# Optimization experiments

Measured on AMD Instinct MI355X. Metric: run time of the kernel, lower is better.

Reference implementation:

```python
import jax, jax.numpy as jnp
from jax import lax
import numpy as np

E = 512        # embedding_dim (= rnn_first hidden, conv kernel, pool kernel)
VOCAB = 50000
H = 512        # hidden_dim of rnn_second
TEMP = 256     # Double_Linear out_feature
NL = 2         # num_layers (rnn_first layers == conv channels == second seq len)
NE = 2         # num_epoches (outer loop in forward)
T = 256        # sentence length
OUT = 1        # out_dim
PAD = (E - 1) // 2                       # 255
CONV_OUT = (E + 2 * PAD - (E - 1) - 1) // 2 + 1   # 256
POOL_OUT = (CONV_OUT + 2 * PAD - (E - 1) - 1) // 2 + 1  # 128 = rnn_second input


def _gru_scan(gi_all, h0, Whh, bhh):
    """PyTorch-convention GRU over precomputed input gates gi_all [T, 3H]."""
    def step(h, gi):
        gh = h @ Whh.T + bhh
        ir, iz, inn = jnp.split(gi, 3)
        hr, hz, hnn = jnp.split(gh, 3)
        r = jax.nn.sigmoid(ir + hr)
        z = jax.nn.sigmoid(iz + hz)
        n = jnp.tanh(inn + r * hnn)
        hn = (1.0 - z) * n + z * h
        return hn, hn
    return lax.scan(step, h0, gi_all)


def setup_inputs() -> dict:
    key = jax.random.key(0)
    ks = jax.random.split(key, 20)
    s = 0.05
    f32 = jnp.float32
    return {
        "sentA": jax.random.randint(ks[0], (T,), 0, VOCAB),
        "sentB": jax.random.randint(ks[1], (T,), 0, VOCAB),
        "emb": jax.random.normal(ks[2], (VOCAB, E), f32),
        "Wih1": jax.random.normal(ks[3], (NL, 3 * E, E), f32) * s,
        "Whh1": jax.random.normal(ks[4], (NL, 3 * E, E), f32) * s,
        "bih1": jax.random.normal(ks[5], (NL, 3 * E), f32) * s,
        "bhh1": jax.random.normal(ks[6], (NL, 3 * E), f32) * s,
        "conv_w": jax.random.normal(ks[7], (NL, NL, E), f32) * s,
        "conv_b": jax.random.normal(ks[8], (NL,), f32) * s,
        "Wih2": jax.random.normal(ks[9], (3 * H, POOL_OUT), f32) * s,
        "Whh2": jax.random.normal(ks[10], (3 * H, H), f32) * s,
        "bih2": jax.random.normal(ks[11], (3 * H,), f32) * s,
        "bhh2": jax.random.normal(ks[12], (3 * H,), f32) * s,
        "WA": jax.random.normal(ks[13], (H, TEMP), f32) * s,
        "WB": jax.random.normal(ks[14], (H, TEMP), f32) * s,
        "b_bi": jax.random.normal(ks[15], (TEMP,), f32) * s,
        "W_lin": jax.random.normal(ks[16], (OUT, TEMP), f32) * s,
        "b_lin": jax.random.normal(ks[17], (OUT,), f32) * s,
    }


def reference(sentA, sentB, emb, Wih1, Whh1, bih1, bhh1, conv_w, conv_b,
              Wih2, Whh2, bih2, bhh2, WA, WB, b_bi, W_lin, b_lin):
    dt = emb.dtype

    def encode(sent):
        h = emb[sent]                                   # [L, E]
        for _ in range(NE):                             # num_epoches loop
            x = h
            finals = []
            for l in range(NL):                         # stacked GRU layers
                gi = x @ Wih1[l].T + bih1[l]            # [L, 3E]
                hT, x = _gru_scan(gi, jnp.zeros((E,), dt), Whh1[l], bhh1[l])
                finals.append(hT)
            h = jnp.stack(finals)                       # hn: [NL, E] -> next seq
        # conv1d (in=out=NL channels, kernel E, stride 2) + maxpool1d
        y = lax.conv_general_dilated(h[None], conv_w, (2,), [(PAD, PAD)],
                                     dimension_numbers=("NCH", "OIH", "NCH"))
        y = y + conv_b[None, :, None]                   # [1, NL, CONV_OUT]
        y = lax.reduce_window(y, -jnp.inf, lax.max, (1, 1, E), (1, 1, 2),
                              [(0, 0), (0, 0), (PAD, PAD)])
        seq = y[0]                                      # [NL, POOL_OUT]
        gi2 = seq @ Wih2.T + bih2                       # [NL, 3H]
        hT, _ = _gru_scan(gi2, jnp.zeros((H,), dt), Whh2, bhh2)
        return hT                                       # [H]

    hA = encode(sentA)
    hB = encode(sentB)
    hx = hA * hB
    hv = jnp.abs(hA - hB)
    hs = hx @ WA + hv @ WB + b_bi                       # Double_Linear
    ht = jnp.tanh(hs)
    out = jax.nn.sigmoid(ht @ W_lin.T + b_lin)
    return out[None]                                    # [1, OUT]
```

## Files before the change

### kernel.cpp

```cpp
#include <hip/hip_runtime.h>
#include <math.h>


__device__ __forceinline__ float sigm(float x) { return 1.f / (1.f + expf(-x)); }

#define LDSP(k) ((k) + (((k) >> 4) << 2))

__device__ __forceinline__ float red32(float v) {
    v += __shfl_xor(v, 16, 64);
    v += __shfl_xor(v, 8, 64);
    v += __shfl_xor(v, 4, 64);
    v += __shfl_xor(v, 2, 64);
    v += __shfl_xor(v, 1, 64);
    return v;
}

__device__ __forceinline__ void poll_ge(const unsigned int* p, unsigned tgt) {
    unsigned v;
    do {
        v = __hip_atomic_load(p, __ATOMIC_RELAXED, __HIP_MEMORY_SCOPE_AGENT);
        if (v < tgt) __builtin_amdgcn_s_sleep(1);
    } while (v < tgt);
}

__device__ __forceinline__ void stage1024(float* dst, const float* src, int tid) {
    if (tid < 256) {
        const unsigned long long* s = (const unsigned long long*)src + tid * 2;
        unsigned long long d0 = __hip_atomic_load(s + 0, __ATOMIC_RELAXED,
                                                  __HIP_MEMORY_SCOPE_AGENT);
        unsigned long long d1 = __hip_atomic_load(s + 1, __ATOMIC_RELAXED,
                                                  __HIP_MEMORY_SCOPE_AGENT);
        union { unsigned long long u; float2 f; } c0, c1;
        c0.u = d0; c1.u = d1;
        float* d = dst + LDSP(tid * 4);
        d[0] = c0.f.x; d[1] = c0.f.y; d[2] = c1.f.x; d[3] = c1.f.y;
    }
}

__device__ __forceinline__ float gru1(float gr, float gz, float gn,
                                      float ar, float az, float an,
                                      const float bh[3], float hp) {
    float r = sigm(gr + ar + bh[0]);
    float z = sigm(gz + az + bh[1]);
    float n = tanhf(gn + r * (an + bh[2]));
    return (1.f - z) * n + z * hp;
}

__global__ __launch_bounds__(512, 1) void k_pipe(
    const float* __restrict__ Whh1, const float* __restrict__ bhh1,
    const float* __restrict__ Wih1, const float* __restrict__ bih1,
    const float* __restrict__ gi0,
    float* __restrict__ e2x,
    float* __restrict__ hbuf0,
    float* __restrict__ hbuf1,
    unsigned int* __restrict__ fL0,
    unsigned int* __restrict__ fL1)
{
    const int tid   = threadIdx.x;
    const int layer = blockIdx.x >> 5;
    const int wgi   = blockIdx.x & 31;
    const int grp   = tid >> 5;
    const int lane  = tid & 31;
    const int j     = wgi * 16 + grp;
    const int colbase = lane * 16;

    __shared__ float xlds[1280];
    __shared__ float hlds[1280];

    const size_t WS = (size_t)1536 * 512;
    const float* WH = Whh1 + (size_t)layer * WS;

    float wh[3][16];
#pragma unroll
    for (int q = 0; q < 3; ++q) {
        const float* src = WH + (size_t)(q * 512 + j) * 512 + colbase;
#pragma unroll
        for (int c4 = 0; c4 < 4; ++c4) {
            float4 v = *(const float4*)(src + c4 * 4);
            wh[q][c4*4+0] = v.x; wh[q][c4*4+1] = v.y;
            wh[q][c4*4+2] = v.z; wh[q][c4*4+3] = v.w;
        }
    }
#pragma unroll
    for (int q = 0; q < 3; ++q)
#pragma unroll
        for (int c = 0; c < 16; ++c)
            asm volatile("" : "+v"(wh[q][c]));

    float bh[3];
#pragma unroll
    for (int q = 0; q < 3; ++q) bh[q] = bhh1[layer * 1536 + q * 512 + j];

    float hprev[2] = {0.f, 0.f};

    if (layer == 0) {
        for (int t = 1; t <= 256; ++t) {
            float g0[3][2];
#pragma unroll
            for (int q = 0; q < 3; ++q)
#pragma unroll
                for (int s = 0; s < 2; ++s)
                    g0[q][s] = gi0[((size_t)(s * 256 + t - 1)) * 1536 + q * 512 + j];

            float acc[3][2] = {{0.f,0.f},{0.f,0.f},{0.f,0.f}};
            if (t > 1) {
                if (tid < 32) poll_ge(fL0 + tid * 16, (unsigned)(t - 1));
                __syncthreads();
                stage1024(xlds, hbuf0 + (size_t)(t - 1) * 1024, tid);
                __syncthreads();
#pragma unroll
                for (int s = 0; s < 2; ++s) {
                    const int base = s * 640 + 20 * lane;
#pragma unroll
                    for (int c4 = 0; c4 < 4; ++c4) {
                        float4 hv = *(const float4*)&xlds[base + c4 * 4];
#pragma unroll
                        for (int q = 0; q < 3; ++q)
                            acc[q][s] += wh[q][c4*4+0]*hv.x + wh[q][c4*4+1]*hv.y
                                       + wh[q][c4*4+2]*hv.z + wh[q][c4*4+3]*hv.w;
                    }
                }
#pragma unroll
                for (int q = 0; q < 3; ++q)
#pragma unroll
                    for (int s = 0; s < 2; ++s) acc[q][s] = red32(acc[q][s]);
            }

            float hn[2];
#pragma unroll
            for (int s = 0; s < 2; ++s) {
                hn[s] = gru1(g0[0][s], g0[1][s], g0[2][s],
                             acc[0][s], acc[1][s], acc[2][s], bh, hprev[s]);
                hprev[s] = hn[s];
            }
            if (lane == 0) {
#pragma unroll
                for (int s = 0; s < 2; ++s) {
                    __hip_atomic_store(hbuf0 + (size_t)t * 1024 + s * 512 + j, hn[s],
                                       __ATOMIC_RELAXED, __HIP_MEMORY_SCOPE_AGENT);
                    if (t == 256) e2x[s * 1024 + j] = hn[s];
                }
            }
            __builtin_amdgcn_s_waitcnt(0);
            __syncthreads();
            if (tid == 0)
                __hip_atomic_store(fL0 + wgi * 16, (unsigned)t,
                                   __ATOMIC_RELAXED, __HIP_MEMORY_SCOPE_AGENT);
        }
    } else {
        const float* WI = Wih1 + WS;
        float wi[3][16];
#pragma unroll
        for (int q = 0; q < 3; ++q) {
            const float* src = WI + (size_t)(q * 512 + j) * 512 + colbase;
#pragma unroll
            for (int c4 = 0; c4 < 4; ++c4) {
                float4 v = *(const float4*)(src + c4 * 4);
                wi[q][c4*4+0] = v.x; wi[q][c4*4+1] = v.y;
                wi[q][c4*4+2] = v.z; wi[q][c4*4+3] = v.w;
            }
        }
#pragma unroll
        for (int q = 0; q < 3; ++q)
#pragma unroll
            for (int c = 0; c < 16; ++c)
                asm volatile("" : "+v"(wi[q][c]));

        float bi[3];
#pragma unroll
        for (int q = 0; q < 3; ++q) bi[q] = bih1[1536 + q * 512 + j];

        for (int t = 1; t <= 256; ++t) {
            if (tid < 32) poll_ge(fL0 + tid * 16, (unsigned)t);
            else if (t > 1 && tid >= 64 && tid < 96)
                poll_ge(fL1 + (tid - 64) * 16, (unsigned)(t - 1));
            __syncthreads();
            stage1024(xlds, hbuf0 + (size_t)t * 1024, tid);
            if (t > 1 && tid >= 256 && tid < 512) {
                const int i = tid - 256;
                const unsigned long long* s =
                    (const unsigned long long*)(hbuf1 + (size_t)(t - 1) * 1024) + i * 2;
                unsigned long long d0 = __hip_atomic_load(s + 0, __ATOMIC_RELAXED,
                                                          __HIP_MEMORY_SCOPE_AGENT);
                unsigned long long d1 = __hip_atomic_load(s + 1, __ATOMIC_RELAXED,
                                                          __HIP_MEMORY_SCOPE_AGENT);
                union { unsigned long long u; float2 f; } c0, c1;
                c0.u = d0; c1.u = d1;
                float* d = hlds + LDSP(i * 4);
                d[0] = c0.f.x; d[1] = c0.f.y; d[2] = c1.f.x; d[3] = c1.f.y;
            }
            __syncthreads();

            float aR[2] = {0.f,0.f}, aZ[2] = {0.f,0.f};
            float aGN[2] = {0.f,0.f}, aHN[2] = {0.f,0.f};
#pragma unroll
            for (int s = 0; s < 2; ++s) {
                const int base = s * 640 + 20 * lane;
#pragma unroll
                for (int c4 = 0; c4 < 4; ++c4) {
                    float4 xv = *(const float4*)&xlds[base + c4 * 4];
                    aR[s]  += wi[0][c4*4+0]*xv.x + wi[0][c4*4+1]*xv.y
                            + wi[0][c4*4+2]*xv.z + wi[0][c4*4+3]*xv.w;
                    aZ[s]  += wi[1][c4*4+0]*xv.x + wi[1][c4*4+1]*xv.y
                            + wi[1][c4*4+2]*xv.z + wi[1][c4*4+3]*xv.w;
                    aGN[s] += wi[2][c4*4+0]*xv.x + wi[2][c4*4+1]*xv.y
                            + wi[2][c4*4+2]*xv.z + wi[2][c4*4+3]*xv.w;
                }
                if (t > 1) {
#pragma unroll
                    for (int c4 = 0; c4 < 4; ++c4) {
                        float4 hv = *(const float4*)&hlds[base + c4 * 4];
                        aR[s]  += wh[0][c4*4+0]*hv.x + wh[0][c4*4+1]*hv.y
                                + wh[0][c4*4+2]*hv.z + wh[0][c4*4+3]*hv.w;
                        aZ[s]  += wh[1][c4*4+0]*hv.x + wh[1][c4*4+1]*hv.y
                                + wh[1][c4*4+2]*hv.z + wh[1][c4*4+3]*hv.w;
                        aHN[s] += wh[2][c4*4+0]*hv.x + wh[2][c4*4+1]*hv.y
                                + wh[2][c4*4+2]*hv.z + wh[2][c4*4+3]*hv.w;
                    }
                }
            }
#pragma unroll
            for (int s = 0; s < 2; ++s) {
                aR[s] = red32(aR[s]); aZ[s] = red32(aZ[s]);
                aGN[s] = red32(aGN[s]); aHN[s] = red32(aHN[s]);
            }

            float hn[2];
#pragma unroll
            for (int s = 0; s < 2; ++s) {
                float r = sigm(aR[s] + bi[0] + bh[0]);
                float z = sigm(aZ[s] + bi[1] + bh[1]);
                float n = tanhf(aGN[s] + bi[2] + r * (aHN[s] + bh[2]));
                hn[s] = (1.f - z) * n + z * hprev[s];
                hprev[s] = hn[s];
            }
            if (lane == 0) {
#pragma unroll
                for (int s = 0; s < 2; ++s) {
                    __hip_atomic_store(hbuf1 + (size_t)t * 1024 + s * 512 + j, hn[s],
                                       __ATOMIC_RELAXED, __HIP_MEMORY_SCOPE_AGENT);
                    if (t == 256) e2x[s * 1024 + 512 + j] = hn[s];
                }
            }
            __builtin_amdgcn_s_waitcnt(0);
            __syncthreads();
            if (tid == 0)
                __hip_atomic_store(fL1 + wgi * 16, (unsigned)t,
                                   __ATOMIC_RELAXED, __HIP_MEMORY_SCOPE_AGENT);
        }
    }
}

__global__ __launch_bounds__(512, 1) void k_tail(
    const float* __restrict__ Wih1, const float* __restrict__ bih1,
    const float* __restrict__ Whh1, const float* __restrict__ bhh1,
    const float* __restrict__ convw, const float* __restrict__ convb,
    const float* __restrict__ Whh2, const float* __restrict__ bhh2,
    const float* __restrict__ bih2, const float* __restrict__ Srow,
    const float* __restrict__ e2x,
    const float* __restrict__ WA, const float* __restrict__ WB,
    const float* __restrict__ b_bi, const float* __restrict__ Wlin,
    const float* __restrict__ blin,
    float* __restrict__ tb0, float* __restrict__ tb1, float* __restrict__ tr,
    float* __restrict__ Mmax,
    unsigned int* __restrict__ tctr, unsigned int* __restrict__ mf,
    float* __restrict__ outp)
{
    const int tid = threadIdx.x;
    const int wgi = blockIdx.x;
    const int grp = tid >> 5, lane = tid & 31;
    const int j = wgi * 16 + grp, colbase = lane * 16;
    const size_t WS = (size_t)1536 * 512;

    __shared__ float xlds[1280];
    __shared__ float hlds[1280];
    __shared__ float red[8];
    __shared__ float smax[4];

#define WAIT_ALL(val)  do { if (tid < 32) poll_ge(tctr + tid * 16, (unsigned)(val)); \
                            __syncthreads(); } while (0)
#define PUBLISH(val)   do { __builtin_amdgcn_s_waitcnt(0); __syncthreads(); \
                            if (tid == 0) __hip_atomic_store(tctr + wgi * 16, (unsigned)(val), \
                                __ATOMIC_RELAXED, __HIP_MEMORY_SCOPE_AGENT); } while (0)

    if (tid < 256) {
        const int i = tid * 4, s = i >> 9, k = i & 511;
        float4 v = *(const float4*)(e2x + s * 1024 + k);
        float* d = xlds + LDSP(i);
        d[0] = v.x; d[1] = v.y; d[2] = v.z; d[3] = v.w;
    } else {
        const int i = (tid - 256) * 4, s = i >> 9, k = i & 511;
        float4 v = *(const float4*)(e2x + s * 1024 + 512 + k);
        float* d = hlds + LDSP(i);
        d[0] = v.x; d[1] = v.y; d[2] = v.z; d[3] = v.w;
    }
    __syncthreads();

    float gp[2][2][3];
    float bh[3], hp[2];
#pragma unroll
    for (int q = 0; q < 3; ++q) {
        const float* wp = Wih1 + (size_t)(q * 512 + j) * 512 + colbase;
        float w16[16];
#pragma unroll
        for (int c4 = 0; c4 < 4; ++c4) {
            float4 v = *(const float4*)(wp + c4 * 4);
            w16[c4*4+0] = v.x; w16[c4*4+1] = v.y; w16[c4*4+2] = v.z; w16[c4*4+3] = v.w;
        }
        float d00 = 0.f, d01 = 0.f, d10 = 0.f, d11 = 0.f;
#pragma unroll
        for (int c = 0; c < 16; ++c) {
            const int b0 = 20 * lane + ((colbase + c) & 15) + 0;
            (void)b0;
        }
#pragma unroll
        for (int c4 = 0; c4 < 4; ++c4) {
            float4 x0 = *(const float4*)&xlds[0 * 640 + 20 * lane + c4 * 4];
            float4 x1 = *(const float4*)&xlds[1 * 640 + 20 * lane + c4 * 4];
            float4 y0 = *(const float4*)&hlds[0 * 640 + 20 * lane + c4 * 4];
            float4 y1 = *(const float4*)&hlds[1 * 640 + 20 * lane + c4 * 4];
            d00 += w16[c4*4+0]*x0.x + w16[c4*4+1]*x0.y + w16[c4*4+2]*x0.z + w16[c4*4+3]*x0.w;
            d01 += w16[c4*4+0]*x1.x + w16[c4*4+1]*x1.y + w16[c4*4+2]*x1.z + w16[c4*4+3]*x1.w;
            d10 += w16[c4*4+0]*y0.x + w16[c4*4+1]*y0.y + w16[c4*4+2]*y0.z + w16[c4*4+3]*y0.w;
            d11 += w16[c4*4+0]*y1.x + w16[c4*4+1]*y1.y + w16[c4*4+2]*y1.z + w16[c4*4+3]*y1.w;
        }
        const float biq = bih1[q * 512 + j];
        gp[0][0][q] = red32(d00) + biq; gp[0][1][q] = red32(d01) + biq;
        gp[1][0][q] = red32(d10) + biq; gp[1][1][q] = red32(d11) + biq;
    }
#pragma unroll
    for (int q = 0; q < 3; ++q) bh[q] = bhh1[q * 512 + j];

#pragma unroll
    for (int s = 0; s < 2; ++s)
        hp[s] = gru1(gp[0][s][0], gp[0][s][1], gp[0][s][2], 0.f, 0.f, 0.f, bh, 0.f);
    if (lane == 0)
#pragma unroll
        for (int s = 0; s < 2; ++s)
            __hip_atomic_store(tb0 + 1024 + s * 512 + j, hp[s],
                               __ATOMIC_RELAXED, __HIP_MEMORY_SCOPE_AGENT);
    PUBLISH(1);

    WAIT_ALL(1);
    stage1024(hlds, tb0 + 1024, tid);
    __syncthreads();
    {
        float wh3[3][16];
#pragma unroll
        for (int q = 0; q < 3; ++q) {
            const float* wp = Whh1 + (size_t)(q * 512 + j) * 512 + colbase;
#pragma unroll
            for (int c4 = 0; c4 < 4; ++c4) {
                float4 v = *(const float4*)(wp + c4 * 4);
                wh3[q][c4*4+0] = v.x; wh3[q][c4*4+1] = v.y;
                wh3[q][c4*4+2] = v.z; wh3[q][c4*4+3] = v.w;
            }
        }
        float acc[3][2] = {{0.f,0.f},{0.f,0.f},{0.f,0.f}};
#pragma unroll
        for (int s = 0; s < 2; ++s) {
            const int base = s * 640 + 20 * lane;
#pragma unroll
            for (int c4 = 0; c4 < 4; ++c4) {
                float4 hv = *(const float4*)&hlds[base + c4 * 4];
#pragma unroll
                for (int q = 0; q < 3; ++q)
                    acc[q][s] += wh3[q][c4*4+0]*hv.x + wh3[q][c4*4+1]*hv.y
                               + wh3[q][c4*4+2]*hv.z + wh3[q][c4*4+3]*hv.w;
            }
        }
#pragma unroll
        for (int s = 0; s < 2; ++s) {
            float a0 = red32(acc[0][s]), a1 = red32(acc[1][s]), a2 = red32(acc[2][s]);
            hp[s] = gru1(gp[1][s][0], gp[1][s][1], gp[1][s][2], a0, a1, a2, bh, hp[s]);
        }
        if (lane == 0)
#pragma unroll
            for (int s = 0; s < 2; ++s)
                __hip_atomic_store(tb0 + 2048 + s * 512 + j, hp[s],
                                   __ATOMIC_RELAXED, __HIP_MEMORY_SCOPE_AGENT);
        PUBLISH(2);
    }

    WAIT_ALL(2);
    stage1024(xlds, tb0 + 1024, tid);
    if (tid >= 256) {
        const int i = tid - 256;
        const unsigned long long* s = (const unsigned long long*)(tb0 + 2048) + i * 2;
        unsigned long long d0 = __hip_atomic_load(s + 0, __ATOMIC_RELAXED, __HIP_MEMORY_SCOPE_AGENT);
        unsigned long long d1 = __hip_atomic_load(s + 1, __ATOMIC_RELAXED, __HIP_MEMORY_SCOPE_AGENT);
        union { unsigned long long u; float2 f; } c0, c1; c0.u = d0; c1.u = d1;
        float* d = hlds + LDSP(i * 4);
        d[0] = c0.f.x; d[1] = c0.f.y; d[2] = c1.f.x; d[3] = c1.f.y;
    }
    __syncthreads();
#pragma unroll
    for (int q = 0; q < 3; ++q) {
        const float* wp = Wih1 + WS + (size_t)(q * 512 + j) * 512 + colbase;
        float w16[16];
#pragma unroll
        for (int c4 = 0; c4 < 4; ++c4) {
            float4 v = *(const float4*)(wp + c4 * 4);
            w16[c4*4+0] = v.x; w16[c4*4+1] = v.y; w16[c4*4+2] = v.z; w16[c4*4+3] = v.w;
        }
        float d00 = 0.f, d01 = 0.f, d10 = 0.f, d11 = 0.f;
#pragma unroll
        for (int c4 = 0; c4 < 4; ++c4) {
            float4 x0 = *(const float4*)&xlds[0 * 640 + 20 * lane + c4 * 4];
            float4 x1 = *(const float4*)&xlds[1 * 640 + 20 * lane + c4 * 4];
            float4 y0 = *(const float4*)&hlds[0 * 640 + 20 * lane + c4 * 4];
            float4 y1 = *(const float4*)&hlds[1 * 640 + 20 * lane + c4 * 4];
            d00 += w16[c4*4+0]*x0.x + w16[c4*4+1]*x0.y + w16[c4*4+2]*x0.z + w16[c4*4+3]*x0.w;
            d01 += w16[c4*4+0]*x1.x + w16[c4*4+1]*x1.y + w16[c4*4+2]*x1.z + w16[c4*4+3]*x1.w;
            d10 += w16[c4*4+0]*y0.x + w16[c4*4+1]*y0.y + w16[c4*4+2]*y0.z + w16[c4*4+3]*y0.w;
            d11 += w16[c4*4+0]*y1.x + w16[c4*4+1]*y1.y + w16[c4*4+2]*y1.z + w16[c4*4+3]*y1.w;
        }
        const float biq = bih1[1536 + q * 512 + j];
        gp[0][0][q] = red32(d00) + biq; gp[0][1][q] = red32(d01) + biq;
        gp[1][0][q] = red32(d10) + biq; gp[1][1][q] = red32(d11) + biq;
    }
#pragma unroll
    for (int q = 0; q < 3; ++q) bh[q] = bhh1[1536 + q * 512 + j];

#pragma unroll
    for (int s = 0; s < 2; ++s)
        hp[s] = gru1(gp[0][s][0], gp[0][s][1], gp[0][s][2], 0.f, 0.f, 0.f, bh, 0.f);
    if (lane == 0)
#pragma unroll
        for (int s = 0; s < 2; ++s)
            __hip_atomic_store(tb1 + 1024 + s * 512 + j, hp[s],
                               __ATOMIC_RELAXED, __HIP_MEMORY_SCOPE_AGENT);
    PUBLISH(3);

    WAIT_ALL(3);
    stage1024(hlds, tb1 + 1024, tid);
    __syncthreads();
    {
        float wh3[3][16];
#pragma unroll
        for (int q = 0; q < 3; ++q) {
            const float* wp = Whh1 + WS + (size_t)(q * 512 + j) * 512 + colbase;
#pragma unroll
            for (int c4 = 0; c4 < 4; ++c4) {
                float4 v = *(const float4*)(wp + c4 * 4);
                wh3[q][c4*4+0] = v.x; wh3[q][c4*4+1] = v.y;
                wh3[q][c4*4+2] = v.z; wh3[q][c4*4+3] = v.w;
            }
        }
        float acc[3][2] = {{0.f,0.f},{0.f,0.f},{0.f,0.f}};
#pragma unroll
        for (int s = 0; s < 2; ++s) {
            const int base = s * 640 + 20 * lane;
#pragma unroll
            for (int c4 = 0; c4 < 4; ++c4) {
                float4 hv = *(const float4*)&hlds[base + c4 * 4];
#pragma unroll
                for (int q = 0; q < 3; ++q)
                    acc[q][s] += wh3[q][c4*4+0]*hv.x + wh3[q][c4*4+1]*hv.y
                               + wh3[q][c4*4+2]*hv.z + wh3[q][c4*4+3]*hv.w;
            }
        }
#pragma unroll
        for (int s = 0; s < 2; ++s) {
            float a0 = red32(acc[0][s]), a1 = red32(acc[1][s]), a2 = red32(acc[2][s]);
            hp[s] = gru1(gp[1][s][0], gp[1][s][1], gp[1][s][2], a0, a1, a2, bh, hp[s]);
        }
        if (lane == 0)
#pragma unroll
            for (int s = 0; s < 2; ++s)
                __hip_atomic_store(tb1 + 2048 + s * 512 + j, hp[s],
                                   __ATOMIC_RELAXED, __HIP_MEMORY_SCOPE_AGENT);
        PUBLISH(4);
    }

    WAIT_ALL(4);
    float m4[4];
    if (wgi == 0) {
        stage1024(xlds, tb0 + 2048, tid);
        if (tid >= 256) {
            const int i = tid - 256;
            const unsigned long long* s = (const unsigned long long*)(tb1 + 2048) + i * 2;
            unsigned long long d0 = __hip_atomic_load(s + 0, __ATOMIC_RELAXED, __HIP_MEMORY_SCOPE_AGENT);
            unsigned long long d1 = __hip_atomic_load(s + 1, __ATOMIC_RELAXED, __HIP_MEMORY_SCOPE_AGENT);
            union { unsigned long long u; float2 f; } c0, c1; c0.u = d0; c1.u = d1;
            float* d = hlds + LDSP(i * 4);
            d[0] = c0.f.x; d[1] = c0.f.y; d[2] = c1.f.x; d[3] = c1.f.y;
        }
        __syncthreads();
        for (int so = 0; so < 4; ++so) {
            const int s = so >> 1, o = so & 1;
            float acc = -3.4e38f;
            if (tid < 256) {
                acc = convb[o];
                const int base = 2 * tid - 255;
                for (int k = 0; k < 512; ++k) {
                    const int pos = base + k;
                    if ((unsigned)pos < 512u) {
                        const int gi0i = s * 512 + pos;
                        acc += xlds[LDSP(gi0i)] * convw[(size_t)(o * 2 + 0) * 512 + k]
                             + hlds[LDSP(gi0i)] * convw[(size_t)(o * 2 + 1) * 512 + k];
                    }
                }
            }
            float m = acc;
            m = fmaxf(m, __shfl_xor(m, 32, 64));
            m = fmaxf(m, __shfl_xor(m, 16, 64));
            m = fmaxf(m, __shfl_xor(m, 8, 64));
            m = fmaxf(m, __shfl_xor(m, 4, 64));
            m = fmaxf(m, __shfl_xor(m, 2, 64));
            m = fmaxf(m, __shfl_xor(m, 1, 64));
            if ((tid & 63) == 0) red[tid >> 6] = m;
            __syncthreads();
            if (tid == 0) {
                float mm = red[0];
                for (int i = 1; i < 8; ++i) mm = fmaxf(mm, red[i]);
                smax[so] = mm;
            }
            __syncthreads();
        }
        if (tid == 0) {
            for (int i = 0; i < 4; ++i)
                __hip_atomic_store(Mmax + i, smax[i],
                                   __ATOMIC_RELAXED, __HIP_MEMORY_SCOPE_AGENT);
            __builtin_amdgcn_s_waitcnt(0);
            __hip_atomic_store(mf, 1u, __ATOMIC_RELAXED, __HIP_MEMORY_SCOPE_AGENT);
        }
        __syncthreads();
#pragma unroll
        for (int i = 0; i < 4; ++i) m4[i] = smax[i];
    } else {
        if (tid == 0) poll_ge(mf, 1u);
        __syncthreads();
#pragma unroll
        for (int i = 0; i < 4; ++i)
            m4[i] = __hip_atomic_load((const float*)Mmax + i, __ATOMIC_RELAXED,
                                      __HIP_MEMORY_SCOPE_AGENT);
    }

    {
        float wh3[3][16];
#pragma unroll
        for (int q = 0; q < 3; ++q) {
            const float* wp = Whh2 + (size_t)(q * 512 + j) * 512 + colbase;
#pragma unroll
            for (int c4 = 0; c4 < 4; ++c4) {
                float4 v = *(const float4*)(wp + c4 * 4);
                wh3[q][c4*4+0] = v.x; wh3[q][c4*4+1] = v.y;
                wh3[q][c4*4+2] = v.z; wh3[q][c4*4+3] = v.w;
            }
        }
#pragma unroll
        for (int q = 0; q < 3; ++q) {
            const float sq = Srow[q * 512 + j];
            const float biq = bih2[q * 512 + j];
#pragma unroll
            for (int s = 0; s < 2; ++s) {
                gp[0][s][q] = m4[s * 2 + 0] * sq + biq;
                gp[1][s][q] = m4[s * 2 + 1] * sq + biq;
            }
            bh[q] = bhh2[q * 512 + j];
        }
#pragma unroll
        for (int s = 0; s < 2; ++s)
            hp[s] = gru1(gp[0][s][0], gp[0][s][1], gp[0][s][2], 0.f, 0.f, 0.f, bh, 0.f);
        if (lane == 0)
#pragma unroll
            for (int s = 0; s < 2; ++s)
                __hip_atomic_store(tr + 1024 + s * 512 + j, hp[s],
                                   __ATOMIC_RELAXED, __HIP_MEMORY_SCOPE_AGENT);
        PUBLISH(5);

        WAIT_ALL(5);
        stage1024(hlds, tr + 1024, tid);
        __syncthreads();
        float acc[3][2] = {{0.f,0.f},{0.f,0.f},{0.f,0.f}};
#pragma unroll
        for (int s = 0; s < 2; ++s) {
            const int base = s * 640 + 20 * lane;
#pragma unroll
            for (int c4 = 0; c4 < 4; ++c4) {
                float4 hv = *(const float4*)&hlds[base + c4 * 4];
#pragma unroll
                for (int q = 0; q < 3; ++q)
                    acc[q][s] += wh3[q][c4*4+0]*hv.x + wh3[q][c4*4+1]*hv.y
                               + wh3[q][c4*4+2]*hv.z + wh3[q][c4*4+3]*hv.w;
            }
        }
#pragma unroll
        for (int s = 0; s < 2; ++s) {
            float a0 = red32(acc[0][s]), a1 = red32(acc[1][s]), a2 = red32(acc[2][s]);
            hp[s] = gru1(gp[1][s][0], gp[1][s][1], gp[1][s][2], a0, a1, a2, bh, hp[s]);
        }
        if (lane == 0)
#pragma unroll
            for (int s = 0; s < 2; ++s)
                __hip_atomic_store(tr + 2048 + s * 512 + j, hp[s],
                                   __ATOMIC_RELAXED, __HIP_MEMORY_SCOPE_AGENT);
        PUBLISH(6);
    }

    WAIT_ALL(6);
    if (wgi != 0) return;
    stage1024(xlds, tr + 2048, tid);
    __syncthreads();
    float v = 0.f;
    if (tid < 256) {
        float acc = b_bi[tid];
        for (int jj = 0; jj < 512; ++jj) {
            const float a = xlds[LDSP(jj)];
            const float b = xlds[LDSP(512 + jj)];
            acc += (a * b) * WA[(size_t)jj * 256 + tid]
                 + fabsf(a - b) * WB[(size_t)jj * 256 + tid];
        }
        v = tanhf(acc) * Wlin[tid];
    }
    v += __shfl_xor(v, 32, 64);
    v += __shfl_xor(v, 16, 64);
    v += __shfl_xor(v, 8, 64);
    v += __shfl_xor(v, 4, 64);
    v += __shfl_xor(v, 2, 64);
    v += __shfl_xor(v, 1, 64);
    if ((tid & 63) == 0) red[tid >> 6] = v;
    __syncthreads();
    if (tid == 0) {
        float ssum = blin[0];
        for (int i = 0; i < 8; ++i) ssum += red[i];
        outp[0] = 1.f / (1.f + expf(-ssum));
    }
#undef WAIT_ALL
#undef PUBLISH
}

__global__ __launch_bounds__(256, 2) void k_gemm_gi(
    const float* __restrict__ W, const float* __restrict__ bias,
    const float* __restrict__ emb, const int* __restrict__ sentA,
    const int* __restrict__ sentB, float* __restrict__ out)
{
    __shared__ float At[32][68];
    __shared__ float Wt[32][68];
    const int tid = threadIdx.x;
    const int n0 = blockIdx.x * 64;
    const int m0 = blockIdx.y * 64;
    const int lrow = tid >> 3, lc4 = tid & 7;

    const int ma = m0 + lrow, mb = ma + 32;
    const int ia = (ma < 256) ? sentA[ma & 255] : sentB[ma & 255];
    const int ib = (mb < 256) ? sentA[mb & 255] : sentB[mb & 255];
    const float* ar0 = emb + (size_t)ia * 512;
    const float* ar1 = emb + (size_t)ib * 512;
    const float* wr0 = W + (size_t)(n0 + lrow) * 512;
    const float* wr1 = wr0 + (size_t)32 * 512;

    const int ty = tid >> 4, tx = tid & 15;
    float acc[4][4];
#pragma unroll
    for (int i = 0; i < 4; ++i)
#pragma unroll
        for (int jj = 0; jj < 4; ++jj) acc[i][jj] = 0.f;

    for (int kk = 0; kk < 512; kk += 32) {
        float4 a0 = *(const float4*)(ar0 + kk + lc4 * 4);
        float4 a1 = *(const float4*)(ar1 + kk + lc4 * 4);
        float4 w0 = *(const float4*)(wr0 + kk + lc4 * 4);
        float4 w1 = *(const float4*)(wr1 + kk + lc4 * 4);
        __syncthreads();
        const int kb = lc4 * 4;
        At[kb+0][lrow] = a0.x; At[kb+1][lrow] = a0.y; At[kb+2][lrow] = a0.z; At[kb+3][lrow] = a0.w;
        At[kb+0][lrow+32] = a1.x; At[kb+1][lrow+32] = a1.y; At[kb+2][lrow+32] = a1.z; At[kb+3][lrow+32] = a1.w;
        Wt[kb+0][lrow] = w0.x; Wt[kb+1][lrow] = w0.y; Wt[kb+2][lrow] = w0.z; Wt[kb+3][lrow] = w0.w;
        Wt[kb+0][lrow+32] = w1.x; Wt[kb+1][lrow+32] = w1.y; Wt[kb+2][lrow+32] = w1.z; Wt[kb+3][lrow+32] = w1.w;
        __syncthreads();
#pragma unroll
        for (int k = 0; k < 32; ++k) {
            float4 av = *(const float4*)&At[k][ty * 4];
            float4 wv = *(const float4*)&Wt[k][tx * 4];
            acc[0][0] += av.x * wv.x; acc[0][1] += av.x * wv.y; acc[0][2] += av.x * wv.z; acc[0][3] += av.x * wv.w;
            acc[1][0] += av.y * wv.x; acc[1][1] += av.y * wv.y; acc[1][2] += av.y * wv.z; acc[1][3] += av.y * wv.w;
            acc[2][0] += av.z * wv.x; acc[2][1] += av.z * wv.y; acc[2][2] += av.z * wv.z; acc[2][3] += av.z * wv.w;
            acc[3][0] += av.w * wv.x; acc[3][1] += av.w * wv.y; acc[3][2] += av.w * wv.z; acc[3][3] += av.w * wv.w;
        }
    }
    float4 b4 = *(const float4*)(bias + n0 + tx * 4);
#pragma unroll
    for (int i = 0; i < 4; ++i) {
        const int m = m0 + ty * 4 + i;
        float4 r;
        r.x = acc[i][0] + b4.x; r.y = acc[i][1] + b4.y;
        r.z = acc[i][2] + b4.z; r.w = acc[i][3] + b4.w;
        *(float4*)(out + (size_t)m * 1536 + n0 + tx * 4) = r;
    }
}

__global__ __launch_bounds__(256) void k_init(
    const float* __restrict__ Wih2, float* __restrict__ Srow,
    unsigned int* __restrict__ flags)
{
    const int g = blockIdx.x * 256 + threadIdx.x;
    if (g < 1536) {
        float s = 0.f;
        for (int k = 0; k < 128; ++k) s += Wih2[(size_t)g * 128 + k];
        Srow[g] = s;
    }
    if (g < 1552) flags[g] = 0u;
}

extern "C" void kernel_launch(void* const* d_in, const int* in_sizes, int n_in,
                              void* d_out, int out_size, void* d_ws, size_t ws_size,
                              hipStream_t stream)
{
    const int*   sentA = (const int*)d_in[0];
    const int*   sentB = (const int*)d_in[1];
    const float* emb   = (const float*)d_in[2];
    const float* Wih1  = (const float*)d_in[3];
    const float* Whh1  = (const float*)d_in[4];
    const float* bih1  = (const float*)d_in[5];
    const float* bhh1  = (const float*)d_in[6];
    const float* convw = (const float*)d_in[7];
    const float* convb = (const float*)d_in[8];
    const float* Wih2  = (const float*)d_in[9];
    const float* Whh2  = (const float*)d_in[10];
    const float* bih2  = (const float*)d_in[11];
    const float* bhh2  = (const float*)d_in[12];
    const float* WA    = (const float*)d_in[13];
    const float* WB    = (const float*)d_in[14];
    const float* b_bi  = (const float*)d_in[15];
    const float* Wlin  = (const float*)d_in[16];
    const float* blin  = (const float*)d_in[17];

    float* ws = (float*)d_ws;
    size_t off = 0;
    float* gi_buf = ws + off; off += 786432;
    float* e2x    = ws + off; off += 2048;
    float* hbuf0  = ws + off; off += 257 * 1024;
    float* hbuf1  = ws + off; off += 257 * 1024;
    float* tb0    = ws + off; off += 3 * 1024;
    float* tb1    = ws + off; off += 3 * 1024;
    float* tr     = ws + off; off += 3 * 1024;
    float* Mmax   = ws + off; off += 16;
    float* Srow   = ws + off; off += 1536;
    unsigned int* flags = (unsigned int*)(ws + off);
    unsigned int* fL0  = flags;
    unsigned int* fL1  = flags + 512;
    unsigned int* tctr = flags + 1024;
    unsigned int* mf   = flags + 1536;

    k_init<<<8, 256, 0, stream>>>(Wih2, Srow, flags);

    k_gemm_gi<<<dim3(24, 8), 256, 0, stream>>>(Wih1, bih1, emb, sentA, sentB, gi_buf);

    k_pipe<<<64, 512, 0, stream>>>(Whh1, bhh1, Wih1, bih1, gi_buf,
                                   e2x, hbuf0, hbuf1, fL0, fL1);

    k_tail<<<32, 512, 0, stream>>>(Wih1, bih1, Whh1, bhh1, convw, convb,
                                   Whh2, bhh2, bih2, Srow, e2x,
                                   WA, WB, b_bi, Wlin, blin,
                                   tb0, tb1, tr, Mmax, tctr, mf, (float*)d_out);
}
```

Measured before the change: 1.360 ms.

## Replace flag-based sync with poisoned-value polling and fuse input GEMM into pipeline

Removes the separate input-gate GEMM kernel: layer 0 now gathers embedding rows and computes its input projection inline using register-resident Wih weights, as layer 1 already did. Per-step flag counters and their extra barriers are replaced by polling the hidden-state buffers directly until no element holds a poison sentinel, which k_init now writes over both buffers. LDS staging is double-buffered so only one barrier per step is needed. Layer 0 does more work per step, and correctness now depends on no computed hidden value ever equalling the sentinel bit pattern (2.0f, which a GRU hidden state bounded in (-1,1) cannot reach).

```diff
diff --git a/kernel.cpp b/kernel.cpp
--- a/kernel.cpp
+++ b/kernel.cpp
@@ -3,6 +3,8 @@
 
 
 __device__ __forceinline__ float sigm(float x) { return 1.f / (1.f + expf(-x)); }
+
+#define POISON_U32 0x40000000u
 
 #define LDSP(k) ((k) + (((k) >> 4) << 2))
 
@@ -21,6 +23,25 @@
         v = __hip_atomic_load(p, __ATOMIC_RELAXED, __HIP_MEMORY_SCOPE_AGENT);
         if (v < tgt) __builtin_amdgcn_s_sleep(1);
     } while (v < tgt);
+}
+
+__device__ __forceinline__ void stage4_poison(float* dstbase, const float* src,
+                                              int idx) {
+    const unsigned long long* sp = (const unsigned long long*)src + idx * 2;
+    unsigned long long d0, d1;
+    for (;;) {
+        d0 = __hip_atomic_load(sp + 0, __ATOMIC_RELAXED, __HIP_MEMORY_SCOPE_AGENT);
+        d1 = __hip_atomic_load(sp + 1, __ATOMIC_RELAXED, __HIP_MEMORY_SCOPE_AGENT);
+        if ((unsigned)(d0 & 0xFFFFFFFFu) != POISON_U32 &&
+            (unsigned)(d0 >> 32)         != POISON_U32 &&
+            (unsigned)(d1 & 0xFFFFFFFFu) != POISON_U32 &&
+            (unsigned)(d1 >> 32)         != POISON_U32) break;
+        __builtin_amdgcn_s_sleep(1);
+    }
+    union { unsigned long long u; float2 f; } c0, c1;
+    c0.u = d0; c1.u = d1;
+    float* d = dstbase + LDSP(idx * 4);
+    d[0] = c0.f.x; d[1] = c0.f.y; d[2] = c1.f.x; d[3] = c1.f.y;
 }
 
 __device__ __forceinline__ void stage1024(float* dst, const float* src, int tid) {
@@ -49,12 +70,11 @@
 __global__ __launch_bounds__(512, 1) void k_pipe(
     const float* __restrict__ Whh1, const float* __restrict__ bhh1,
     const float* __restrict__ Wih1, const float* __restrict__ bih1,
-    const float* __restrict__ gi0,
+    const float* __restrict__ emb,
+    const int* __restrict__ sentA, const int* __restrict__ sentB,
     float* __restrict__ e2x,
     float* __restrict__ hbuf0,
-    float* __restrict__ hbuf1,
-    unsigned int* __restrict__ fL0,
-    unsigned int* __restrict__ fL1)
+    float* __restrict__ hbuf1)
 {
     const int tid   = threadIdx.x;
     const int layer = blockIdx.x >> 5;
@@ -64,189 +84,116 @@
     const int j     = wgi * 16 + grp;
     const int colbase = lane * 16;
 
-    __shared__ float xlds[1280];
-    __shared__ float hlds[1280];
+    __shared__ float xl[2][1280];
+    __shared__ float hl[2][1280];
 
     const size_t WS = (size_t)1536 * 512;
     const float* WH = Whh1 + (size_t)layer * WS;
-
-    float wh[3][16];
+    const float* WI = Wih1 + (size_t)layer * WS;
+
+    float wh[3][16], wi[3][16];
 #pragma unroll
     for (int q = 0; q < 3; ++q) {
-        const float* src = WH + (size_t)(q * 512 + j) * 512 + colbase;
+        const float* srcH = WH + (size_t)(q * 512 + j) * 512 + colbase;
+        const float* srcI = WI + (size_t)(q * 512 + j) * 512 + colbase;
 #pragma unroll
         for (int c4 = 0; c4 < 4; ++c4) {
-            float4 v = *(const float4*)(src + c4 * 4);
-            wh[q][c4*4+0] = v.x; wh[q][c4*4+1] = v.y;
-            wh[q][c4*4+2] = v.z; wh[q][c4*4+3] = v.w;
+            float4 vH = *(const float4*)(srcH + c4 * 4);
+            float4 vI = *(const float4*)(srcI + c4 * 4);
+            wh[q][c4*4+0] = vH.x; wh[q][c4*4+1] = vH.y;
+            wh[q][c4*4+2] = vH.z; wh[q][c4*4+3] = vH.w;
+            wi[q][c4*4+0] = vI.x; wi[q][c4*4+1] = vI.y;
+            wi[q][c4*4+2] = vI.z; wi[q][c4*4+3] = vI.w;
         }
     }
 #pragma unroll
     for (int q = 0; q < 3; ++q)
 #pragma unroll
-        for (int c = 0; c < 16; ++c)
+        for (int c = 0; c < 16; ++c) {
             asm volatile("" : "+v"(wh[q][c]));
-
-    float bh[3];
-#pragma unroll
-    for (int q = 0; q < 3; ++q) bh[q] = bhh1[layer * 1536 + q * 512 + j];
-
+            asm volatile("" : "+v"(wi[q][c]));
+        }
+
+    float bh[3], bi[3];
+#pragma unroll
+    for (int q = 0; q < 3; ++q) {
+        bh[q] = bhh1[layer * 1536 + q * 512 + j];
+        bi[q] = bih1[layer * 1536 + q * 512 + j];
+    }
+
+    float* hout = (layer == 0) ? hbuf0 : hbuf1;
     float hprev[2] = {0.f, 0.f};
 
-    if (layer == 0) {
-        for (int t = 1; t <= 256; ++t) {
-            float g0[3][2];
-#pragma unroll
-            for (int q = 0; q < 3; ++q)
-#pragma unroll
-                for (int s = 0; s < 2; ++s)
-                    g0[q][s] = gi0[((size_t)(s * 256 + t - 1)) * 1536 + q * 512 + j];
-
-            float acc[3][2] = {{0.f,0.f},{0.f,0.f},{0.f,0.f}};
+    for (int t = 1; t <= 256; ++t) {
+        const int p = t & 1;
+
+        if (tid < 256) {
+            if (layer == 0) {
+                const int i = tid * 4, s = i >> 9, k = i & 511;
+                const int idx = s ? sentB[t - 1] : sentA[t - 1];
+                float4 v = *(const float4*)(emb + (size_t)idx * 512 + k);
+                float* d = &xl[p][LDSP(i)];
+                d[0] = v.x; d[1] = v.y; d[2] = v.z; d[3] = v.w;
+            } else {
+                stage4_poison(xl[p], hbuf0 + (size_t)t * 1024, tid);
+            }
+        } else if (t > 1) {
+            stage4_poison(hl[p], hout + (size_t)(t - 1) * 1024, tid - 256);
+        }
+        __syncthreads();
+
+        float aR[2] = {0.f,0.f}, aZ[2] = {0.f,0.f};
+        float aGN[2] = {0.f,0.f}, aHN[2] = {0.f,0.f};
+#pragma unroll
+        for (int s = 0; s < 2; ++s) {
+            const int base = s * 640 + 20 * lane;
+#pragma unroll
+            for (int c4 = 0; c4 < 4; ++c4) {
+                float4 xv = *(const float4*)&xl[p][base + c4 * 4];
+                aR[s]  += wi[0][c4*4+0]*xv.x + wi[0][c4*4+1]*xv.y
+                        + wi[0][c4*4+2]*xv.z + wi[0][c4*4+3]*xv.w;
+                aZ[s]  += wi[1][c4*4+0]*xv.x + wi[1][c4*4+1]*xv.y
+                        + wi[1][c4*4+2]*xv.z + wi[1][c4*4+3]*xv.w;
+                aGN[s] += wi[2][c4*4+0]*xv.x + wi[2][c4*4+1]*xv.y
+                        + wi[2][c4*4+2]*xv.z + wi[2][c4*4+3]*xv.w;
+            }
             if (t > 1) {
-                if (tid < 32) poll_ge(fL0 + tid * 16, (unsigned)(t - 1));
-                __syncthreads();
-                stage1024(xlds, hbuf0 + (size_t)(t - 1) * 1024, tid);
-                __syncthreads();
-#pragma unroll
-                for (int s = 0; s < 2; ++s) {
-                    const int base = s * 640 + 20 * lane;
-#pragma unroll
-                    for (int c4 = 0; c4 < 4; ++c4) {
-                        float4 hv = *(const float4*)&xlds[base + c4 * 4];
-#pragma unroll
-                        for (int q = 0; q < 3; ++q)
-                            acc[q][s] += wh[q][c4*4+0]*hv.x + wh[q][c4*4+1]*hv.y
-                                       + wh[q][c4*4+2]*hv.z + wh[q][c4*4+3]*hv.w;
-                    }
+#pragma unroll
+                for (int c4 = 0; c4 < 4; ++c4) {
+                    float4 hv = *(const float4*)&hl[p][base + c4 * 4];
+                    aR[s]  += wh[0][c4*4+0]*hv.x + wh[0][c4*4+1]*hv.y
+                            + wh[0][c4*4+2]*hv.z + wh[0][c4*4+3]*hv.w;
+                    aZ[s]  += wh[1][c4*4+0]*hv.x + wh[1][c4*4+1]*hv.y
+                            + wh[1][c4*4+2]*hv.z + wh[1][c4*4+3]*hv.w;
+                    aHN[s] += wh[2][c4*4+0]*hv.x + wh[2][c4*4+1]*hv.y
+                            + wh[2][c4*4+2]*hv.z + wh[2][c4*4+3]*hv.w;
                 }
-#pragma unroll
-                for (int q = 0; q < 3; ++q)
-#pragma unroll
-                    for (int s = 0; s < 2; ++s) acc[q][s] = red32(acc[q][s]);
-            }
-
-            float hn[2];
+            }
+        }
+#pragma unroll
+        for (int s = 0; s < 2; ++s) {
+            aR[s] = red32(aR[s]); aZ[s] = red32(aZ[s]);
+            aGN[s] = red32(aGN[s]); aHN[s] = red32(aHN[s]);
+        }
+
+        float hn[2];
+#pragma unroll
+        for (int s = 0; s < 2; ++s) {
+            float r = sigm(aR[s] + bi[0] + bh[0]);
+            float z = sigm(aZ[s] + bi[1] + bh[1]);
+            float n = tanhf(aGN[s] + bi[2] + r * (aHN[s] + bh[2]));
+            hn[s] = (1.f - z) * n + z * hprev[s];
+            hprev[s] = hn[s];
+        }
+
+        if (lane == 0) {
 #pragma unroll
             for (int s = 0; s < 2; ++s) {
-                hn[s] = gru1(g0[0][s], g0[1][s], g0[2][s],
-                             acc[0][s], acc[1][s], acc[2][s], bh, hprev[s]);
-                hprev[s] = hn[s];
-            }
-            if (lane == 0) {
-#pragma unroll
-                for (int s = 0; s < 2; ++s) {
-                    __hip_atomic_store(hbuf0 + (size_t)t * 1024 + s * 512 + j, hn[s],
-                                       __ATOMIC_RELAXED, __HIP_MEMORY_SCOPE_AGENT);
-                    if (t == 256) e2x[s * 1024 + j] = hn[s];
-                }
-            }
-            __builtin_amdgcn_s_waitcnt(0);
-            __syncthreads();
-            if (tid == 0)
-                __hip_atomic_store(fL0 + wgi * 16, (unsigned)t,
+                __hip_atomic_store(hout + (size_t)t * 1024 + s * 512 + j, hn[s],
                                    __ATOMIC_RELAXED, __HIP_MEMORY_SCOPE_AGENT);
-        }
-    } else {
-        const float* WI = Wih1 + WS;
-        float wi[3][16];
-#pragma unroll
-        for (int q = 0; q < 3; ++q) {
-            const float* src = WI + (size_t)(q * 512 + j) * 512 + colbase;
-#pragma unroll
-            for (int c4 = 0; c4 < 4; ++c4) {
-                float4 v = *(const float4*)(src + c4 * 4);
-                wi[q][c4*4+0] = v.x; wi[q][c4*4+1] = v.y;
-                wi[q][c4*4+2] = v.z; wi[q][c4*4+3] = v.w;
-            }
-        }
-#pragma unroll
-        for (int q = 0; q < 3; ++q)
-#pragma unroll
-            for (int c = 0; c < 16; ++c)
-                asm volatile("" : "+v"(wi[q][c]));
-
-        float bi[3];
-#pragma unroll
-        for (int q = 0; q < 3; ++q) bi[q] = bih1[1536 + q * 512 + j];
-
-        for (int t = 1; t <= 256; ++t) {
-            if (tid < 32) poll_ge(fL0 + tid * 16, (unsigned)t);
-            else if (t > 1 && tid >= 64 && tid < 96)
-                poll_ge(fL1 + (tid - 64) * 16, (unsigned)(t - 1));
-            __syncthreads();
-            stage1024(xlds, hbuf0 + (size_t)t * 1024, tid);
-            if (t > 1 && tid >= 256 && tid < 512) {
-                const int i = tid - 256;
-                const unsigned long long* s =
-                    (const unsigned long long*)(hbuf1 + (size_t)(t - 1) * 1024) + i * 2;
-                unsigned long long d0 = __hip_atomic_load(s + 0, __ATOMIC_RELAXED,
-                                                          __HIP_MEMORY_SCOPE_AGENT);
-                unsigned long long d1 = __hip_atomic_load(s + 1, __ATOMIC_RELAXED,
-                                                          __HIP_MEMORY_SCOPE_AGENT);
-                union { unsigned long long u; float2 f; } c0, c1;
-                c0.u = d0; c1.u = d1;
-                float* d = hlds + LDSP(i * 4);
-                d[0] = c0.f.x; d[1] = c0.f.y; d[2] = c1.f.x; d[3] = c1.f.y;
-            }
-            __syncthreads();
-
-            float aR[2] = {0.f,0.f}, aZ[2] = {0.f,0.f};
-            float aGN[2] = {0.f,0.f}, aHN[2] = {0.f,0.f};
-#pragma unroll
-            for (int s = 0; s < 2; ++s) {
-                const int base = s * 640 + 20 * lane;
-#pragma unroll
-                for (int c4 = 0; c4 < 4; ++c4) {
-                    float4 xv = *(const float4*)&xlds[base + c4 * 4];
-                    aR[s]  += wi[0][c4*4+0]*xv.x + wi[0][c4*4+1]*xv.y
-                            + wi[0][c4*4+2]*xv.z + wi[0][c4*4+3]*xv.w;
-                    aZ[s]  += wi[1][c4*4+0]*xv.x + wi[1][c4*4+1]*xv.y
-                            + wi[1][c4*4+2]*xv.z + wi[1][c4*4+3]*xv.w;
-                    aGN[s] += wi[2][c4*4+0]*xv.x + wi[2][c4*4+1]*xv.y
-                            + wi[2][c4*4+2]*xv.z + wi[2][c4*4+3]*xv.w;
-                }
-                if (t > 1) {
-#pragma unroll
-                    for (int c4 = 0; c4 < 4; ++c4) {
-                        float4 hv = *(const float4*)&hlds[base + c4 * 4];
-                        aR[s]  += wh[0][c4*4+0]*hv.x + wh[0][c4*4+1]*hv.y
-                                + wh[0][c4*4+2]*hv.z + wh[0][c4*4+3]*hv.w;
-                        aZ[s]  += wh[1][c4*4+0]*hv.x + wh[1][c4*4+1]*hv.y
-                                + wh[1][c4*4+2]*hv.z + wh[1][c4*4+3]*hv.w;
-                        aHN[s] += wh[2][c4*4+0]*hv.x + wh[2][c4*4+1]*hv.y
-                                + wh[2][c4*4+2]*hv.z + wh[2][c4*4+3]*hv.w;
-                    }
-                }
-            }
-#pragma unroll
-            for (int s = 0; s < 2; ++s) {
-                aR[s] = red32(aR[s]); aZ[s] = red32(aZ[s]);
-                aGN[s] = red32(aGN[s]); aHN[s] = red32(aHN[s]);
-            }
-
-            float hn[2];
-#pragma unroll
-            for (int s = 0; s < 2; ++s) {
-                float r = sigm(aR[s] + bi[0] + bh[0]);
-                float z = sigm(aZ[s] + bi[1] + bh[1]);
-                float n = tanhf(aGN[s] + bi[2] + r * (aHN[s] + bh[2]));
-                hn[s] = (1.f - z) * n + z * hprev[s];
-                hprev[s] = hn[s];
-            }
-            if (lane == 0) {
-#pragma unroll
-                for (int s = 0; s < 2; ++s) {
-                    __hip_atomic_store(hbuf1 + (size_t)t * 1024 + s * 512 + j, hn[s],
-                                       __ATOMIC_RELAXED, __HIP_MEMORY_SCOPE_AGENT);
-                    if (t == 256) e2x[s * 1024 + 512 + j] = hn[s];
-                }
-            }
-            __builtin_amdgcn_s_waitcnt(0);
-            __syncthreads();
-            if (tid == 0)
-                __hip_atomic_store(fL1 + wgi * 16, (unsigned)t,
-                                   __ATOMIC_RELAXED, __HIP_MEMORY_SCOPE_AGENT);
+                if (t == 256)
+                    e2x[s * 1024 + layer * 512 + j] = hn[s];
+            }
         }
     }
 }
@@ -309,11 +256,6 @@
         }
         float d00 = 0.f, d01 = 0.f, d10 = 0.f, d11 = 0.f;
 #pragma unroll
-        for (int c = 0; c < 16; ++c) {
-            const int b0 = 20 * lane + ((colbase + c) & 15) + 0;
-            (void)b0;
-        }
-#pragma unroll
         for (int c4 = 0; c4 < 4; ++c4) {
             float4 x0 = *(const float4*)&xlds[0 * 640 + 20 * lane + c4 * 4];
             float4 x1 = *(const float4*)&xlds[1 * 640 + 20 * lane + c4 * 4];
@@ -631,68 +573,9 @@
 #undef PUBLISH
 }
 
-__global__ __launch_bounds__(256, 2) void k_gemm_gi(
-    const float* __restrict__ W, const float* __restrict__ bias,
-    const float* __restrict__ emb, const int* __restrict__ sentA,
-    const int* __restrict__ sentB, float* __restrict__ out)
-{
-    __shared__ float At[32][68];
-    __shared__ float Wt[32][68];
-    const int tid = threadIdx.x;
-    const int n0 = blockIdx.x * 64;
-    const int m0 = blockIdx.y * 64;
-    const int lrow = tid >> 3, lc4 = tid & 7;
-
-    const int ma = m0 + lrow, mb = ma + 32;
-    const int ia = (ma < 256) ? sentA[ma & 255] : sentB[ma & 255];
-    const int ib = (mb < 256) ? sentA[mb & 255] : sentB[mb & 255];
-    const float* ar0 = emb + (size_t)ia * 512;
-    const float* ar1 = emb + (size_t)ib * 512;
-    const float* wr0 = W + (size_t)(n0 + lrow) * 512;
-    const float* wr1 = wr0 + (size_t)32 * 512;
-
-    const int ty = tid >> 4, tx = tid & 15;
-    float acc[4][4];
-#pragma unroll
-    for (int i = 0; i < 4; ++i)
-#pragma unroll
-        for (int jj = 0; jj < 4; ++jj) acc[i][jj] = 0.f;
-
-    for (int kk = 0; kk < 512; kk += 32) {
-        float4 a0 = *(const float4*)(ar0 + kk + lc4 * 4);
-        float4 a1 = *(const float4*)(ar1 + kk + lc4 * 4);
-        float4 w0 = *(const float4*)(wr0 + kk + lc4 * 4);
-        float4 w1 = *(const float4*)(wr1 + kk + lc4 * 4);
-        __syncthreads();
-        const int kb = lc4 * 4;
-        At[kb+0][lrow] = a0.x; At[kb+1][lrow] = a0.y; At[kb+2][lrow] = a0.z; At[kb+3][lrow] = a0.w;
-        At[kb+0][lrow+32] = a1.x; At[kb+1][lrow+32] = a1.y; At[kb+2][lrow+32] = a1.z; At[kb+3][lrow+32] = a1.w;
-        Wt[kb+0][lrow] = w0.x; Wt[kb+1][lrow] = w0.y; Wt[kb+2][lrow] = w0.z; Wt[kb+3][lrow] = w0.w;
-        Wt[kb+0][lrow+32] = w1.x; Wt[kb+1][lrow+32] = w1.y; Wt[kb+2][lrow+32] = w1.z; Wt[kb+3][lrow+32] = w1.w;
-        __syncthreads();
-#pragma unroll
-        for (int k = 0; k < 32; ++k) {
-            float4 av = *(const float4*)&At[k][ty * 4];
-            float4 wv = *(const float4*)&Wt[k][tx * 4];
-            acc[0][0] += av.x * wv.x; acc[0][1] += av.x * wv.y; acc[0][2] += av.x * wv.z; acc[0][3] += av.x * wv.w;
-            acc[1][0] += av.y * wv.x; acc[1][1] += av.y * wv.y; acc[1][2] += av.y * wv.z; acc[1][3] += av.y * wv.w;
-            acc[2][0] += av.z * wv.x; acc[2][1] += av.z * wv.y; acc[2][2] += av.z * wv.z; acc[2][3] += av.z * wv.w;
-            acc[3][0] += av.w * wv.x; acc[3][1] += av.w * wv.y; acc[3][2] += av.w * wv.z; acc[3][3] += av.w * wv.w;
-        }
-    }
-    float4 b4 = *(const float4*)(bias + n0 + tx * 4);
-#pragma unroll
-    for (int i = 0; i < 4; ++i) {
-        const int m = m0 + ty * 4 + i;
-        float4 r;
-        r.x = acc[i][0] + b4.x; r.y = acc[i][1] + b4.y;
-        r.z = acc[i][2] + b4.z; r.w = acc[i][3] + b4.w;
-        *(float4*)(out + (size_t)m * 1536 + n0 + tx * 4) = r;
-    }
-}
-
 __global__ __launch_bounds__(256) void k_init(
     const float* __restrict__ Wih2, float* __restrict__ Srow,
+    unsigned int* __restrict__ hbufs,
     unsigned int* __restrict__ flags)
 {
     const int g = blockIdx.x * 256 + threadIdx.x;
@@ -701,7 +584,13 @@
         for (int k = 0; k < 128; ++k) s += Wih2[(size_t)g * 128 + k];
         Srow[g] = s;
     }
-    if (g < 1552) flags[g] = 0u;
+    const int NBIG = 257 * 1024;
+    const int NTOT = 2 * NBIG;
+    for (int i = g; i < NTOT; i += gridDim.x * 256) {
+        const int off = (i < NBIG) ? i : i - NBIG;
+        hbufs[i] = (off < 1024) ? 0u : POISON_U32;
+    }
+    if (g < 528) flags[g] = 0u;
 }
 
 extern "C" void kernel_launch(void* const* d_in, const int* in_sizes, int n_in,
@@ -729,7 +618,6 @@
 
     float* ws = (float*)d_ws;
     size_t off = 0;
-    float* gi_buf = ws + off; off += 786432;
     float* e2x    = ws + off; off += 2048;
     float* hbuf0  = ws + off; off += 257 * 1024;
     float* hbuf1  = ws + off; off += 257 * 1024;
@@ -739,17 +627,13 @@
     float* Mmax   = ws + off; off += 16;
     float* Srow   = ws + off; off += 1536;
     unsigned int* flags = (unsigned int*)(ws + off);
-    unsigned int* fL0  = flags;
-    unsigned int* fL1  = flags + 512;
-    unsigned int* tctr = flags + 1024;
-    unsigned int* mf   = flags + 1536;
-
-    k_init<<<8, 256, 0, stream>>>(Wih2, Srow, flags);
-
-    k_gemm_gi<<<dim3(24, 8), 256, 0, stream>>>(Wih1, bih1, emb, sentA, sentB, gi_buf);
-
-    k_pipe<<<64, 512, 0, stream>>>(Whh1, bhh1, Wih1, bih1, gi_buf,
-                                   e2x, hbuf0, hbuf1, fL0, fL1);
+    unsigned int* tctr = flags;
+    unsigned int* mf   = flags + 512;
+
+    k_init<<<256, 256, 0, stream>>>(Wih2, Srow, (unsigned int*)hbuf0, flags);
+
+    k_pipe<<<64, 512, 0, stream>>>(Whh1, bhh1, Wih1, bih1, emb, sentA, sentB,
+                                   e2x, hbuf0, hbuf1);
 
     k_tail<<<32, 512, 0, stream>>>(Wih1, bih1, Whh1, bhh1, convw, convb,
                                    Whh2, bhh2, bih2, Srow, e2x,
```

After: 1.494 ms. 1.1x slower.
